# Optimization experiments

Measured on AMD Instinct MI355X. Metric: run time of the kernel, lower is better.

## Reference

```python
import jax, jax.numpy as jnp
import numpy as np

EMBED_DIM = 64  # scale factor dim (matches head dim)


def setup_inputs() -> dict:
    key0 = jax.random.key(0)
    kq, kk, kv = jax.random.split(key0, 3)
    shape = (2, 16, 2048, 64)  # [B, H, S, D]
    return {
        "query": jax.random.normal(kq, shape, dtype=jnp.float32),
        "key": jax.random.normal(kk, shape, dtype=jnp.float32),
        "value": jax.random.normal(kv, shape, dtype=jnp.float32),
    }


def reference(query, key, value):
    # qk = Q K^T / sqrt(embed_dim); softmax over last dim; @ V
    inv_scale = jnp.sqrt(jnp.asarray(EMBED_DIM, dtype=query.dtype))
    scores = jnp.einsum("bhqd,bhkd->bhqk", query, key) / inv_scale
    probs = jax.nn.softmax(scores, axis=-1)
    # dropout_p=0.0 -> identity (eval semantics)
    return jnp.einsum("bhqk,bhkd->bhqd", probs, value)
```

## Files before the change

### kernel.cpp

```cpp
#include <hip/hip_runtime.h>
#include <hip/hip_bf16.h>

#define S_LEN 2048
#define DDIM  64
#define NT    (S_LEN / 64)
#define SCALE  0.125f
#define SCALE2 0.18033688f
#define NELEM  4194304
#define NQROW  65536
#define WC_LGKM0 0xc07f

typedef __attribute__((ext_vector_type(8))) short short8;
typedef __attribute__((ext_vector_type(4))) short short4v;
typedef __attribute__((ext_vector_type(4))) float floatx4;

__device__ __forceinline__ short f2bf(float f) {
    union { float f; unsigned u; } v; v.f = f;
    return (short)((v.u + 0x7fffu + ((v.u >> 16) & 1u)) >> 16);
}

__device__ __forceinline__ unsigned pk2bf(float a, float b) {
#if __has_builtin(__builtin_amdgcn_cvt_pk_bf16_f32)
    auto r = __builtin_amdgcn_cvt_pk_bf16_f32(a, b);
    union { decltype(r) v; unsigned u; } c; c.v = r; return c.u;
#else
    union { float f; unsigned u; } x, y; x.f = a; y.f = b;
    unsigned lo = (x.u + 0x7fffu + ((x.u >> 16) & 1u)) >> 16;
    unsigned hi = (y.u + 0x7fffu + ((y.u >> 16) & 1u)) & 0xffff0000u;
    return lo | hi;
#endif
}

__device__ __forceinline__ float fexp2(float x) {
#if __has_builtin(__builtin_amdgcn_exp2f)
    return __builtin_amdgcn_exp2f(x);
#else
    return exp2f(x);
#endif
}

__global__ __launch_bounds__(256) void prep_kv(const float* __restrict__ K,
                                               const float* __restrict__ V,
                                               short* __restrict__ Kb,
                                               short* __restrict__ Vt) {
    const int bh = blockIdx.x & 31;
    const int st = blockIdx.x >> 5;
    const int t  = threadIdx.x;
    const size_t tile_off = (size_t)bh * (S_LEN * DDIM) + (size_t)st * (64 * DDIM);

    {
        const float* src = K + tile_off + t * 16;
        short* dst = Kb + tile_off + t * 16;
        #pragma unroll
        for (int h = 0; h < 2; ++h) {
            float4 a = *(const float4*)(src + h * 8);
            float4 b = *(const float4*)(src + h * 8 + 4);
            uint4 o;
            o.x = pk2bf(a.x, a.y); o.y = pk2bf(a.z, a.w);
            o.z = pk2bf(b.x, b.y); o.w = pk2bf(b.z, b.w);
            *(uint4*)(dst + h * 8) = o;
        }
    }

    {
        const int s4 = (t & 15) * 4;
        const int d4 = (t >> 4) * 4;
        const float* src = V + tile_off;
        float4 v0 = *(const float4*)(src + (size_t)(s4 + 0) * 64 + d4);
        float4 v1 = *(const float4*)(src + (size_t)(s4 + 1) * 64 + d4);
        float4 v2 = *(const float4*)(src + (size_t)(s4 + 2) * 64 + d4);
        float4 v3 = *(const float4*)(src + (size_t)(s4 + 3) * 64 + d4);
        const float* r0 = (const float*)&v0;
        const float* r1 = (const float*)&v1;
        const float* r2 = (const float*)&v2;
        const float* r3 = (const float*)&v3;
        short* dstb = Vt + (size_t)bh * (DDIM * S_LEN) + (size_t)st * 64 + s4;
        #pragma unroll
        for (int dd = 0; dd < 4; ++dd) {
            uint2 o;
            o.x = pk2bf(r0[dd], r1[dd]);
            o.y = pk2bf(r2[dd], r3[dd]);
            *(uint2*)(dstb + (size_t)(d4 + dd) * S_LEN) = o;
        }
    }
}

template <int NSPLIT>
__global__ __launch_bounds__(256) void attn_sm(
    const float* __restrict__ Q, const short* __restrict__ Kb,
    const short* __restrict__ Vt, float* __restrict__ O,
    float* __restrict__ numer, float* __restrict__ denom)
{
    __shared__ short Ks[64 * 64];
    __shared__ short Vs[64 * 64];
    __shared__ short Pl[4][32 * 64];

    constexpr int NIT = NT / NSPLIT;

    const int tid  = threadIdx.x;
    const int wave = tid >> 6;
    const int lane = tid & 63;
    const int l16  = lane & 15;
    const int quad = lane >> 4;
    const int x7   = l16 & 7;

    const int bh = blockIdx.x & 31;
    const int rest = blockIdx.x >> 5;
    const int qt = rest & 15;
    const int ks = rest >> 4;
    const size_t base = (size_t)bh * (S_LEN * DDIM);

    const int ci0 = tid,        r0 = ci0 >> 3, c0 = (ci0 & 7) ^ (r0 & 7);
    const int ci1 = 256 + tid,  r1 = ci1 >> 3, c1 = (ci1 & 7) ^ (r1 & 7);
    const size_t koff = (size_t)ks * NIT * (64 * 64);
    const size_t voff = (size_t)ks * NIT * 64;
    const short* pK0 = Kb + base + koff + r0 * 64 + c0 * 8;
    const short* pK1 = Kb + base + koff + r1 * 64 + c1 * 8;
    const short* pV0 = Vt + base + voff + (size_t)r0 * S_LEN + c0 * 8;
    const short* pV1 = Vt + base + voff + (size_t)r1 * S_LEN + c1 * 8;

    short8 rk0 = *(const short8*)pK0;
    short8 rk1 = *(const short8*)pK1;
    short8 rv0 = *(const short8*)pV0;
    short8 rv1 = *(const short8*)pV1;

    short8 qf[2][2];
    #pragma unroll
    for (int nq = 0; nq < 2; ++nq) {
        const float* qp = Q + base + (size_t)(qt * 128 + wave * 32 + nq * 16 + l16) * 64 + quad * 8;
        #pragma unroll
        for (int kt = 0; kt < 2; ++kt) {
            float4 a = *(const float4*)(qp + kt * 32);
            float4 b = *(const float4*)(qp + kt * 32 + 4);
            union { unsigned u[4]; short8 s; } qc;
            qc.u[0] = pk2bf(a.x * SCALE2, a.y * SCALE2);
            qc.u[1] = pk2bf(a.z * SCALE2, a.w * SCALE2);
            qc.u[2] = pk2bf(b.x * SCALE2, b.y * SCALE2);
            qc.u[3] = pk2bf(b.z * SCALE2, b.w * SCALE2);
            qf[nq][kt] = qc.s;
        }
    }

    floatx4 oacc[2][4];
    float rs[2];
    #pragma unroll
    for (int mt = 0; mt < 2; ++mt) {
        #pragma unroll
        for (int dt = 0; dt < 4; ++dt) oacc[mt][dt] = (floatx4){0.f,0.f,0.f,0.f};
        rs[mt] = 0.f;
    }

    short* Pw = &Pl[wave][0];

    for (int kb = 0; kb < NIT; ++kb) {
        if (kb) __builtin_amdgcn_s_barrier();

        *(short8*)&Ks[ci0 * 8] = rk0;
        *(short8*)&Ks[ci1 * 8] = rk1;
        *(short8*)&Vs[ci0 * 8] = rv0;
        *(short8*)&Vs[ci1 * 8] = rv1;

        if (kb + 1 < NIT) {
            const int ok = (kb + 1) * (64 * 64), ov = (kb + 1) * 64;
            rk0 = *(const short8*)(pK0 + ok);
            rk1 = *(const short8*)(pK1 + ok);
            rv0 = *(const short8*)(pV0 + ov);
            rv1 = *(const short8*)(pV1 + ov);
        }

        __builtin_amdgcn_s_waitcnt(WC_LGKM0);
        __builtin_amdgcn_s_barrier();

        floatx4 sc[2][4];
        #pragma unroll
        for (int mk = 0; mk < 4; ++mk) {
            floatx4 a0 = (floatx4){0.f,0.f,0.f,0.f};
            floatx4 a1 = (floatx4){0.f,0.f,0.f,0.f};
            #pragma unroll
            for (int kt = 0; kt < 2; ++kt) {
                const int csw = (kt * 4 + quad) ^ x7;
                short8 kf = *(const short8*)&Ks[(mk * 16 + l16) * 64 + csw * 8];
                a0 = __builtin_amdgcn_mfma_f32_16x16x32_bf16(kf, qf[0][kt], a0, 0, 0, 0);
                a1 = __builtin_amdgcn_mfma_f32_16x16x32_bf16(kf, qf[1][kt], a1, 0, 0, 0);
            }
            sc[0][mk] = a0; sc[1][mk] = a1;
        }

        #pragma unroll
        for (int nq = 0; nq < 2; ++nq) {
            const int prow = (nq * 16 + l16) * 64;
            #pragma unroll
            for (int mk = 0; mk < 4; ++mk) {
                float p0 = fexp2(sc[nq][mk][0]);
                float p1 = fexp2(sc[nq][mk][1]);
                float p2 = fexp2(sc[nq][mk][2]);
                float p3 = fexp2(sc[nq][mk][3]);
                rs[nq] += (p0 + p1) + (p2 + p3);
                uint2 pv; pv.x = pk2bf(p0, p1); pv.y = pk2bf(p2, p3);
                const int c8 = (mk * 4 + quad) ^ (2 * x7);
                *(uint2*)&Pw[prow + c8 * 4] = pv;
            }
        }

        #pragma unroll
        for (int kt = 0; kt < 2; ++kt) {
            const int csw = (kt * 4 + quad) ^ x7;
            short8 pf0 = *(const short8*)&Pw[(l16)      * 64 + csw * 8];
            short8 pf1 = *(const short8*)&Pw[(16 + l16) * 64 + csw * 8];
            #pragma unroll
            for (int dt = 0; dt < 4; ++dt) {
                short8 vf = *(const short8*)&Vs[(dt * 16 + l16) * 64 + csw * 8];
                oacc[0][dt] = __builtin_amdgcn_mfma_f32_16x16x32_bf16(pf0, vf, oacc[0][dt], 0, 0, 0);
                oacc[1][dt] = __builtin_amdgcn_mfma_f32_16x16x32_bf16(pf1, vf, oacc[1][dt], 0, 0, 0);
            }
        }
    }

    float inv[2];
    #pragma unroll
    for (int nq = 0; nq < 2; ++nq) {
        float s = rs[nq];
        s += __shfl_xor(s, 16, 64);
        s += __shfl_xor(s, 32, 64);
        if (NSPLIT == 2) {
            if (quad == 0)
                denom[(size_t)ks * NQROW + bh * S_LEN + qt * 128 + wave * 32 + nq * 16 + l16] = s;
        }
        inv[nq] = 1.0f / s;
    }

    #pragma unroll
    for (int mt = 0; mt < 2; ++mt) {
        #pragma unroll
        for (int r = 0; r < 4; ++r) {
            const int row = qt * 128 + wave * 32 + mt * 16 + quad * 4 + r;
            if (NSPLIT == 1) {
                const float d_r = __shfl(inv[mt], quad * 4 + r, 64);
                float* op = O + base + (size_t)row * 64 + l16;
                #pragma unroll
                for (int dt = 0; dt < 4; ++dt)
                    op[dt * 16] = oacc[mt][dt][r] * d_r;
            } else {
                float* np = numer + (size_t)ks * NELEM + base + (size_t)row * 64 + l16;
                #pragma unroll
                for (int dt = 0; dt < 4; ++dt)
                    np[dt * 16] = oacc[mt][dt][r];
            }
        }
    }
}

__global__ __launch_bounds__(256) void combine2(const float* __restrict__ numer,
                                                const float* __restrict__ denom,
                                                float* __restrict__ O) {
    const size_t i = ((size_t)blockIdx.x * 256 + threadIdx.x) * 4;
    const size_t q = i >> 6;
    const float inv = 1.0f / (denom[q] + denom[NQROW + q]);
    float4 n0 = *(const float4*)(numer + i);
    float4 n1 = *(const float4*)(numer + NELEM + i);
    float4 o;
    o.x = (n0.x + n1.x) * inv;
    o.y = (n0.y + n1.y) * inv;
    o.z = (n0.z + n1.z) * inv;
    o.w = (n0.w + n1.w) * inv;
    *(float4*)(O + i) = o;
}

#define BQ    64
#define BKEY  64
#define KPAD  72

__global__ __launch_bounds__(256) void attn_kernel(
    const float* __restrict__ Q, const float* __restrict__ K,
    const float* __restrict__ V, float* __restrict__ O)
{
    __shared__ short Ksh[BKEY * KPAD];
    __shared__ short Vtt[DDIM * KPAD];
    __shared__ short Pls[4][16 * KPAD];

    const int tid  = threadIdx.x;
    const int wave = tid >> 6;
    const int lane = tid & 63;
    const int l16  = lane & 15;
    const int quad = lane >> 4;

    const int bh = blockIdx.x & 31;
    const int qt = blockIdx.x >> 5;
    const size_t base = (size_t)bh * S_LEN * DDIM;

    const int qrow = qt * BQ + wave * 16 + l16;
    short8 qf[2];
    {
        const float* qp = Q + base + (size_t)qrow * DDIM + quad * 8;
        #pragma unroll
        for (int kt = 0; kt < 2; ++kt) {
            float4 a = *(const float4*)(qp + kt * 32);
            float4 b = *(const float4*)(qp + kt * 32 + 4);
            short* d = (short*)&qf[kt];
            d[0]=f2bf(a.x*SCALE); d[1]=f2bf(a.y*SCALE); d[2]=f2bf(a.z*SCALE); d[3]=f2bf(a.w*SCALE);
            d[4]=f2bf(b.x*SCALE); d[5]=f2bf(b.y*SCALE); d[6]=f2bf(b.z*SCALE); d[7]=f2bf(b.w*SCALE);
        }
    }

    float m_i[4], l_i[4];
    floatx4 oacc[4];
    #pragma unroll
    for (int r = 0; r < 4; ++r) { m_i[r] = -3.0e38f; l_i[r] = 0.f; }
    #pragma unroll
    for (int dt = 0; dt < 4; ++dt) oacc[dt] = (floatx4){0.f, 0.f, 0.f, 0.f};

    const int skey = tid >> 2;
    const int scol = (tid & 3) * 4;

    for (int kb = 0; kb < S_LEN / BKEY; ++kb) {
        const float* Kg = K + base + (size_t)kb * BKEY * DDIM + (size_t)skey * DDIM;
        const float* Vg = V + base + (size_t)kb * BKEY * DDIM + (size_t)skey * DDIM;
        #pragma unroll
        for (int i = 0; i < 4; ++i) {
            const int c = scol + i * 16;
            float4 kv = *(const float4*)(Kg + c);
            short* kd = &Ksh[skey * KPAD + c];
            kd[0]=f2bf(kv.x); kd[1]=f2bf(kv.y); kd[2]=f2bf(kv.z); kd[3]=f2bf(kv.w);
            float4 vv = *(const float4*)(Vg + c);
            Vtt[(c+0)*KPAD + skey] = f2bf(vv.x);
            Vtt[(c+1)*KPAD + skey] = f2bf(vv.y);
            Vtt[(c+2)*KPAD + skey] = f2bf(vv.z);
            Vtt[(c+3)*KPAD + skey] = f2bf(vv.w);
        }
        __syncthreads();

        floatx4 sc[4];
        #pragma unroll
        for (int nt = 0; nt < 4; ++nt) {
            floatx4 acc = (floatx4){0.f, 0.f, 0.f, 0.f};
            #pragma unroll
            for (int kt = 0; kt < 2; ++kt) {
                short8 kf = *(const short8*)&Ksh[(nt*16 + l16) * KPAD + kt*32 + quad*8];
                acc = __builtin_amdgcn_mfma_f32_16x16x32_bf16(qf[kt], kf, acc, 0, 0, 0);
            }
            sc[nt] = acc;
        }

        short* Pw = &Pls[wave][0];
        #pragma unroll
        for (int r = 0; r < 4; ++r) {
            float mx = fmaxf(fmaxf(sc[0][r], sc[1][r]), fmaxf(sc[2][r], sc[3][r]));
            #pragma unroll
            for (int off = 1; off < 16; off <<= 1)
                mx = fmaxf(mx, __shfl_xor(mx, off, 64));
            const float mnew  = fmaxf(m_i[r], mx);
            const float alpha = __expf(m_i[r] - mnew);
            m_i[r] = mnew;
            float rsum = 0.f;
            #pragma unroll
            for (int nt = 0; nt < 4; ++nt) {
                float p = __expf(sc[nt][r] - mnew);
                rsum += p;
                Pw[(quad*4 + r) * KPAD + nt*16 + l16] = f2bf(p);
            }
            #pragma unroll
            for (int off = 1; off < 16; off <<= 1)
                rsum += __shfl_xor(rsum, off, 64);
            l_i[r] = l_i[r] * alpha + rsum;
            oacc[0][r] *= alpha; oacc[1][r] *= alpha;
            oacc[2][r] *= alpha; oacc[3][r] *= alpha;
        }

        #pragma unroll
        for (int kt = 0; kt < 2; ++kt) {
            short8 pf = *(const short8*)&Pw[l16 * KPAD + kt*32 + quad*8];
            #pragma unroll
            for (int dt = 0; dt < 4; ++dt) {
                short8 vf = *(const short8*)&Vtt[(dt*16 + l16) * KPAD + kt*32 + quad*8];
                oacc[dt] = __builtin_amdgcn_mfma_f32_16x16x32_bf16(pf, vf, oacc[dt], 0, 0, 0);
            }
        }
        __syncthreads();
    }

    #pragma unroll
    for (int r = 0; r < 4; ++r) {
        const float inv = 1.0f / l_i[r];
        const int row = qt * BQ + wave * 16 + quad * 4 + r;
        float* op = O + base + (size_t)row * DDIM + l16;
        #pragma unroll
        for (int dt = 0; dt < 4; ++dt)
            op[dt * 16] = oacc[dt][r] * inv;
    }
}

extern "C" void kernel_launch(void* const* d_in, const int* in_sizes, int n_in,
                              void* d_out, int out_size, void* d_ws, size_t ws_size,
                              hipStream_t stream) {
    const float* Q = (const float*)d_in[0];
    const float* K = (const float*)d_in[1];
    const float* V = (const float*)d_in[2];
    float* O = (float*)d_out;

    const size_t prep_bytes = (size_t)NELEM * 2 * 2;
    const size_t split_bytes = prep_bytes + (size_t)2 * NELEM * 4
                             + (size_t)2 * NQROW * 4;

    if (ws_size >= split_bytes) {
        short* Kb  = (short*)d_ws;
        short* Vtp = (short*)d_ws + NELEM;
        float* num = (float*)((char*)d_ws + prep_bytes);
        float* den = num + (size_t)2 * NELEM;
        prep_kv<<<dim3(1024), dim3(256), 0, stream>>>(K, V, Kb, Vtp);
        attn_sm<2><<<dim3(1024), dim3(256), 0, stream>>>(Q, Kb, Vtp, nullptr, num, den);
        combine2<<<dim3(NELEM / 1024), dim3(256), 0, stream>>>(num, den, O);
    } else if (ws_size >= prep_bytes) {
        short* Kb  = (short*)d_ws;
        short* Vtp = (short*)d_ws + NELEM;
        prep_kv<<<dim3(1024), dim3(256), 0, stream>>>(K, V, Kb, Vtp);
        attn_sm<1><<<dim3(512), dim3(256), 0, stream>>>(Q, Kb, Vtp, O, nullptr, nullptr);
    } else {
        attn_kernel<<<dim3(1024), dim3(256), 0, stream>>>(Q, K, V, O);
    }
}
```

Measured before the change: 151.5 us.

## Load K and V MFMA fragments directly from global memory, dropping LDS staging

Removes the shared-memory staging of K and V tiles, along with the register prefetch and the two block barriers per iteration. Each wave now loads its MFMA operand fragments straight from global memory (through the caches). This cuts LDS traffic and synchronisation, but the four waves each fetch the same K/V tile redundantly and lose the software prefetch that overlapped load latency with compute.

```diff
diff --git a/kernel.cpp b/kernel.cpp
--- a/kernel.cpp
+++ b/kernel.cpp
@@ -8,10 +8,8 @@
 #define SCALE2 0.18033688f
 #define NELEM  4194304
 #define NQROW  65536
-#define WC_LGKM0 0xc07f
 
 typedef __attribute__((ext_vector_type(8))) short short8;
-typedef __attribute__((ext_vector_type(4))) short short4v;
 typedef __attribute__((ext_vector_type(4))) float floatx4;
 
 __device__ __forceinline__ short f2bf(float f) {
@@ -91,8 +89,6 @@
     const short* __restrict__ Vt, float* __restrict__ O,
     float* __restrict__ numer, float* __restrict__ denom)
 {
-    __shared__ short Ks[64 * 64];
-    __shared__ short Vs[64 * 64];
     __shared__ short Pl[4][32 * 64];
 
     constexpr int NIT = NT / NSPLIT;
@@ -110,19 +106,19 @@
     const int ks = rest >> 4;
     const size_t base = (size_t)bh * (S_LEN * DDIM);
 
-    const int ci0 = tid,        r0 = ci0 >> 3, c0 = (ci0 & 7) ^ (r0 & 7);
-    const int ci1 = 256 + tid,  r1 = ci1 >> 3, c1 = (ci1 & 7) ^ (r1 & 7);
-    const size_t koff = (size_t)ks * NIT * (64 * 64);
-    const size_t voff = (size_t)ks * NIT * 64;
-    const short* pK0 = Kb + base + koff + r0 * 64 + c0 * 8;
-    const short* pK1 = Kb + base + koff + r1 * 64 + c1 * 8;
-    const short* pV0 = Vt + base + voff + (size_t)r0 * S_LEN + c0 * 8;
-    const short* pV1 = Vt + base + voff + (size_t)r1 * S_LEN + c1 * 8;
-
-    short8 rk0 = *(const short8*)pK0;
-    short8 rk1 = *(const short8*)pK1;
-    short8 rv0 = *(const short8*)pV0;
-    short8 rv1 = *(const short8*)pV1;
+    const short* pKm[4];
+    const short* pVd[4];
+    {
+        const short* kf0 = Kb + base + (size_t)ks * NIT * (64 * 64)
+                         + (size_t)l16 * 64 + quad * 8;
+        const short* vf0 = Vt + base + (size_t)l16 * S_LEN
+                         + (size_t)ks * NIT * 64 + quad * 8;
+        #pragma unroll
+        for (int i = 0; i < 4; ++i) {
+            pKm[i] = kf0 + i * (16 * 64);
+            pVd[i] = vf0 + (size_t)i * 16 * S_LEN;
+        }
+    }
 
     short8 qf[2][2];
     #pragma unroll
@@ -153,23 +149,8 @@
     short* Pw = &Pl[wave][0];
 
     for (int kb = 0; kb < NIT; ++kb) {
-        if (kb) __builtin_amdgcn_s_barrier();
-
-        *(short8*)&Ks[ci0 * 8] = rk0;
-        *(short8*)&Ks[ci1 * 8] = rk1;
-        *(short8*)&Vs[ci0 * 8] = rv0;
-        *(short8*)&Vs[ci1 * 8] = rv1;
-
-        if (kb + 1 < NIT) {
-            const int ok = (kb + 1) * (64 * 64), ov = (kb + 1) * 64;
-            rk0 = *(const short8*)(pK0 + ok);
-            rk1 = *(const short8*)(pK1 + ok);
-            rv0 = *(const short8*)(pV0 + ov);
-            rv1 = *(const short8*)(pV1 + ov);
-        }
-
-        __builtin_amdgcn_s_waitcnt(WC_LGKM0);
-        __builtin_amdgcn_s_barrier();
+        const int ko = kb * (64 * 64);
+        const int vo = kb * 64;
 
         floatx4 sc[2][4];
         #pragma unroll
@@ -178,8 +159,7 @@
             floatx4 a1 = (floatx4){0.f,0.f,0.f,0.f};
             #pragma unroll
             for (int kt = 0; kt < 2; ++kt) {
-                const int csw = (kt * 4 + quad) ^ x7;
-                short8 kf = *(const short8*)&Ks[(mk * 16 + l16) * 64 + csw * 8];
+                short8 kf = *(const short8*)(pKm[mk] + ko + kt * 32);
                 a0 = __builtin_amdgcn_mfma_f32_16x16x32_bf16(kf, qf[0][kt], a0, 0, 0, 0);
                 a1 = __builtin_amdgcn_mfma_f32_16x16x32_bf16(kf, qf[1][kt], a1, 0, 0, 0);
             }
@@ -209,7 +189,7 @@
             short8 pf1 = *(const short8*)&Pw[(16 + l16) * 64 + csw * 8];
             #pragma unroll
             for (int dt = 0; dt < 4; ++dt) {
-                short8 vf = *(const short8*)&Vs[(dt * 16 + l16) * 64 + csw * 8];
+                short8 vf = *(const short8*)(pVd[dt] + vo + kt * 32);
                 oacc[0][dt] = __builtin_amdgcn_mfma_f32_16x16x32_bf16(pf0, vf, oacc[0][dt], 0, 0, 0);
                 oacc[1][dt] = __builtin_amdgcn_mfma_f32_16x16x32_bf16(pf1, vf, oacc[1][dt], 0, 0, 0);
             }
```

New measurement: 220.7 us. 1.46x slower.
